# Kernel optimization log

Measured on AMD Instinct MI355X. Metric: run time of the kernel, lower is better.

Reference implementation:

```python
import jax, jax.numpy as jnp
import numpy as np
from jax import lax

B, T, D, H = 32, 512, 1024, 1024


def setup_inputs() -> dict:
    key = jax.random.key(0)
    ks = jax.random.split(key, 6)
    inp = jax.random.normal(ks[0], (B, T, D), jnp.float32)
    attention_mask = jnp.ones((B, T), jnp.float32)
    nonzero_index = jax.random.randint(ks[1], (B, 1), 0, T)
    # Stacked gate weights, gate order (i, f, g, o); equivalent to 8 separate Linears.
    W_x = jax.random.normal(ks[2], (D, 4 * H), jnp.float32) * 0.02
    W_h = jax.random.normal(ks[3], (H, 4 * H), jnp.float32) * 0.02
    b_x = jax.random.normal(ks[4], (4 * H,), jnp.float32) * 0.02
    b_h = jax.random.normal(ks[5], (4 * H,), jnp.float32) * 0.02
    return {"input": inp, "attention_mask": attention_mask, "nonzero_index": nonzero_index,
            "W_x": W_x, "W_h": W_h, "b_x": b_x, "b_h": b_h}


def reference(input, attention_mask, nonzero_index, W_x, W_h, b_x, b_h):
    # Precompute all input-side gate projections in one big matmul: [B,T,4H]
    x_gates = jnp.einsum('btd,dg->btg', input, W_x) + b_x + b_h

    def step(carry, xg):
        h, c = carry                       # [B,H] each
        g = xg + h @ W_h                   # [B,4H]
        i, f, gg, o = jnp.split(g, 4, axis=-1)
        i = jax.nn.sigmoid(i)
        f = jax.nn.sigmoid(f)
        gg = jnp.tanh(gg)
        o = jax.nn.sigmoid(o)
        c = f * c + i * gg
        h = o * jnp.tanh(c)
        return (h, c), (h, c)

    h0 = jnp.zeros((B, H), x_gates.dtype)
    c0 = jnp.zeros((B, H), x_gates.dtype)
    _, (hs, cs) = lax.scan(step, (h0, c0), jnp.swapaxes(x_gates, 0, 1))  # [T,B,H]
    hts = jnp.swapaxes(hs, 0, 1)  # [B,T,H]
    cts = jnp.swapaxes(cs, 0, 1)
    # cls token gathered BEFORE masking (matches original order)
    cls_token = jnp.take_along_axis(hts, nonzero_index[:, :, None], axis=1)[:, 0, :]
    hts = hts * attention_mask[:, :, None]
    cts = cts * attention_mask[:, :, None]
    return (hts, hts, cts, cls_token)
```

## Files before the change

kernel.cpp:

```cpp
#include <hip/hip_runtime.h>
#include <stdint.h>


typedef _Float16 f16;
typedef __attribute__((ext_vector_type(8))) _Float16 f16x8;
typedef __attribute__((ext_vector_type(4))) float f32x4;
typedef __attribute__((ext_vector_type(4))) unsigned int u32x4;

#define NG 2
#define NW 8
#define HBYTES (2 * NG * 2048 * 16)

__device__ __forceinline__ float sigm(float v){ return 1.f/(1.f+__expf(-v)); }
__device__ __forceinline__ float tanh_(float v){ return 2.f/(1.f+__expf(-2.f*v)) - 1.f; }

__device__ __forceinline__ u32x4 ld16_sc(const void* p) {
  u32x4 r;
  asm volatile("global_load_dwordx4 %0, %1, off sc0 sc1" : "=v"(r) : "v"(p));
  return r;
}
__device__ __forceinline__ void st2_sc(void* p, uint32_t v) {
  asm volatile("global_store_short %0, %1, off sc0 sc1" :: "v"(p), "v"(v) : "memory");
}

__global__ __launch_bounds__(512, 1) void lstm_kernel(
    const float* __restrict__ xin, const float* __restrict__ amask,
    const int* __restrict__ nzidx, const float* __restrict__ Wx,
    const float* __restrict__ Wh, const float* __restrict__ bx,
    const float* __restrict__ bh, float* __restrict__ out,
    uint32_t* __restrict__ ws)
{
  __shared__ __align__(16) f16 Wl[128][64][8];
  __shared__ __align__(16) float pl[NW][2][64][4];

  const int tid  = threadIdx.x;
  const int lane = tid & 63;
  const int wid  = tid >> 6;
  const int r    = blockIdx.x & 127;
  const int G    = blockIdx.x >> 7;
  const int hbase = r * 8;

  uint8_t* hb8 = (uint8_t*)ws;

  for (int f = wid; f < 128; f += NW) {
    const int side = f >> 6, kf = (f >> 1) & 31, nt = f & 1;
    const int c16 = lane & 15, kslot = lane >> 4;
    const int g = nt * 2 + (c16 >> 3);
    const int gcol = g * 1024 + hbase + (c16 & 7);
    const int k0 = kf * 32 + kslot * 8;
    const float* Wsrc = side ? Wh : Wx;
    f16x8 v;
#pragma unroll
    for (int e = 0; e < 8; ++e) v[e] = (f16)Wsrc[(size_t)(k0 + e) * 4096 + gcol];
    *(f16x8*)&Wl[f][lane][0] = v;
  }
  const int b  = tid >> 3;
  const int hc = tid & 7;
  const int b_glob = G * 16 + b;
  float bias[4] = {0.f, 0.f, 0.f, 0.f};
  float cval = 0.f;
  int myidx = -1;
  if (tid < 128) {
#pragma unroll
    for (int g = 0; g < 4; ++g) {
      const int gcol = g * 1024 + hbase + hc;
      bias[g] = bx[gcol] + bh[gcol];
    }
    myidx = nzidx[b_glob];
  }
  const int bb = lane & 15, kslot = lane >> 4;
  f32x4 xf[4][2];
  {
    const size_t xrow = ((size_t)(G * 16 + bb) * 512) * 1024;
#pragma unroll
    for (int q = 0; q < 4; ++q) {
      const float* xs = xin + xrow + (wid * 4 + q) * 32 + kslot * 8;
      xf[q][0] = *(const f32x4*)xs;
      xf[q][1] = *(const f32x4*)(xs + 4);
    }
  }
  __syncthreads();

  bool gave_up = false;
#pragma unroll 1
  for (int t = 0; t < 512; ++t) {
    f16x8 xa[4];
#pragma unroll
    for (int q = 0; q < 4; ++q) {
      f16x8 a;
#pragma unroll
      for (int i = 0; i < 4; ++i) { a[i] = (f16)xf[q][0][i]; a[i + 4] = (f16)xf[q][1][i]; }
      xa[q] = a;
    }
    f32x4 acc0 = {0.f,0.f,0.f,0.f}, acc1 = {0.f,0.f,0.f,0.f};
#pragma unroll
    for (int q = 0; q < 4; ++q) {
      const int kf = wid * 4 + q;
      f16x8 b0 = *(const f16x8*)&Wl[kf * 2 + 0][lane][0];
      f16x8 b1 = *(const f16x8*)&Wl[kf * 2 + 1][lane][0];
      acc0 = __builtin_amdgcn_mfma_f32_16x16x32_f16(xa[q], b0, acc0, 0, 0, 0);
      acc1 = __builtin_amdgcn_mfma_f32_16x16x32_f16(xa[q], b1, acc1, 0, 0, 0);
    }
    if (t + 1 < 512) {
      const size_t xrow = ((size_t)(G * 16 + bb) * 512 + (size_t)(t + 1)) * 1024;
#pragma unroll
      for (int q = 0; q < 4; ++q) {
        const float* xs = xin + xrow + (wid * 4 + q) * 32 + kslot * 8;
        xf[q][0] = *(const f32x4*)xs;
        xf[q][1] = *(const f32x4*)(xs + 4);
      }
    }
    if (t > 0) {
      const uint8_t* hsrc = hb8 + ((size_t)((t & 1) * NG + G) << 15);
      const uint32_t tb = ((uint32_t)(t >> 1) + 1u) & 3u;
      const uint32_t pat = (tb & 1u) | ((tb >> 1) << 16);
      u32x4 hq[4];
      int spins = 0;
      for (;;) {
#pragma unroll
        for (int q = 0; q < 4; ++q) {
          const int rsrc = (wid * 4 + q) * 4 + kslot;
          hq[q] = ld16_sc(hsrc + ((size_t)(rsrc * 16 + bb) << 4));
        }
        asm volatile("s_waitcnt vmcnt(0)" ::: "memory");
        if (gave_up) break;
        bool ok = true;
#pragma unroll
        for (int q = 0; q < 4; ++q) {
#pragma unroll
          for (int j = 0; j < 4; ++j) ok &= ((hq[q][j] & 0x00010001u) == pat);
        }
        if (__all((int)ok)) break;
        if (++spins > (1 << 13)) { gave_up = true; break; }
        __builtin_amdgcn_s_sleep(1);
      }
#pragma unroll
      for (int q = 0; q < 4; ++q) {
        union { u32x4 u; f16x8 v; } cu; cu.u = hq[q];
        const int kf = wid * 4 + q;
        f16x8 b0 = *(const f16x8*)&Wl[64 + kf * 2 + 0][lane][0];
        f16x8 b1 = *(const f16x8*)&Wl[64 + kf * 2 + 1][lane][0];
        acc0 = __builtin_amdgcn_mfma_f32_16x16x32_f16(cu.v, b0, acc0, 0, 0, 0);
        acc1 = __builtin_amdgcn_mfma_f32_16x16x32_f16(cu.v, b1, acc1, 0, 0, 0);
      }
    }
    *(f32x4*)&pl[wid][0][lane][0] = acc0;
    *(f32x4*)&pl[wid][1][lane][0] = acc1;
    __syncthreads();
    if (tid < 128) {
      float s[4];
#pragma unroll
      for (int g = 0; g < 4; ++g) {
        const int lp = ((g & 1) * 8 + hc) + 16 * (b >> 2);
        const int reg = b & 3;
        float v = bias[g];
#pragma unroll
        for (int w = 0; w < NW; ++w) v += pl[w][g >> 1][lp][reg];
        s[g] = v;
      }
      const float ig = sigm(s[0]);
      const float fg = sigm(s[1]);
      const float gg = tanh_(s[2]);
      const float og = sigm(s[3]);
      cval = fg * cval + ig * gg;
      const float hval = og * tanh_(cval);
      if (t < 511) {
        union { f16 f; uint16_t u; } pk; pk.f = (f16)hval;
        const uint32_t tbp = ((uint32_t)((t + 1) >> 1) + 1u) & 3u;
        const uint32_t bitv = (hc & 1) ? ((tbp >> 1) & 1u) : (tbp & 1u);
        const uint32_t val = ((uint32_t)pk.u & 0xFFFEu) | bitv;
        uint8_t* dst = hb8 + ((size_t)(((t + 1) & 1) * NG + G) << 15)
                     + ((size_t)(r * 16 + b) << 4) + (hc << 1);
        st2_sc(dst, val);
      }
      const float mval = amask[(size_t)b_glob * 512 + (size_t)t];
      const size_t o0 = ((size_t)b_glob * 512 + (size_t)t) * 1024 + (size_t)(hbase + hc);
      out[o0] = hval * mval;
      out[o0 + 16777216u] = hval * mval;
      out[o0 + 33554432u] = cval * mval;
      if (t == myidx) out[50331648u + (size_t)b_glob * 1024 + (size_t)(hbase + hc)] = hval;
    }
    __syncthreads();
  }
}

extern "C" void kernel_launch(void* const* d_in, const int* in_sizes, int n_in,
                              void* d_out, int out_size, void* d_ws, size_t ws_size,
                              hipStream_t stream) {
  const float* xin   = (const float*)d_in[0];
  const float* amask = (const float*)d_in[1];
  const int*   nzidx = (const int*)d_in[2];
  const float* Wx    = (const float*)d_in[3];
  const float* Wh    = (const float*)d_in[4];
  const float* bx    = (const float*)d_in[5];
  const float* bh    = (const float*)d_in[6];
  float* out = (float*)d_out;
  uint32_t* ws = (uint32_t*)d_ws;

  hipMemsetAsync(d_ws, 0, HBYTES, stream);

  void* args[] = {(void*)&xin, (void*)&amask, (void*)&nzidx, (void*)&Wx,
                  (void*)&Wh, (void*)&bx, (void*)&bh, (void*)&out, (void*)&ws};
  hipError_t e = hipLaunchCooperativeKernel((const void*)lstm_kernel, dim3(256), dim3(512),
                                            args, 0, stream);
  if (e != hipSuccess) {
    lstm_kernel<<<dim3(256), dim3(512), 0, stream>>>(xin, amask, nzidx, Wx, Wh, bx, bh, out, ws);
  }
}
```

Baseline: 2.231 ms.

## Double-buffer partial sums, drop trailing barrier, issue h loads before x-side MFMAs

Double-buffers the LDS partial-sum array so the second __syncthreads per step can be removed. The recurrent h loads are issued before the input-side MFMAs so their latency overlaps that compute. The spin loop drops s_sleep and only re-issues loads after a failed check. The next x prefetch now runs after h arrives, and the attention-mask value is prefetched one step ahead. The aim is to shorten the per-step critical path of the serial recurrence, at the cost of tighter polling and more reliance on the flag protocol for ordering.

Result: faster. 2.098 ms (-6.0%).

```diff
diff --git a/kernel.cpp b/kernel.cpp
--- a/kernel.cpp
+++ b/kernel.cpp
@@ -31,7 +31,7 @@
     uint32_t* __restrict__ ws)
 {
   __shared__ __align__(16) f16 Wl[128][64][8];
-  __shared__ __align__(16) float pl[NW][2][64][4];
+  __shared__ __align__(16) float pl[2][NW][2][64][4];
 
   const int tid  = threadIdx.x;
   const int lane = tid & 63;
@@ -44,10 +44,10 @@
 
   for (int f = wid; f < 128; f += NW) {
     const int side = f >> 6, kf = (f >> 1) & 31, nt = f & 1;
-    const int c16 = lane & 15, kslot = lane >> 4;
+    const int c16 = lane & 15, kslot_ = lane >> 4;
     const int g = nt * 2 + (c16 >> 3);
     const int gcol = g * 1024 + hbase + (c16 & 7);
-    const int k0 = kf * 32 + kslot * 8;
+    const int k0 = kf * 32 + kslot_ * 8;
     const float* Wsrc = side ? Wh : Wx;
     f16x8 v;
 #pragma unroll
@@ -58,7 +58,7 @@
   const int hc = tid & 7;
   const int b_glob = G * 16 + b;
   float bias[4] = {0.f, 0.f, 0.f, 0.f};
-  float cval = 0.f;
+  float cval = 0.f, mv_cur = 0.f;
   int myidx = -1;
   if (tid < 128) {
 #pragma unroll
@@ -67,6 +67,7 @@
       bias[g] = bx[gcol] + bh[gcol];
     }
     myidx = nzidx[b_glob];
+    mv_cur = amask[(size_t)b_glob * 512];
   }
   const int bb = lane & 15, kslot = lane >> 4;
   f32x4 xf[4][2];
@@ -84,6 +85,7 @@
   bool gave_up = false;
 #pragma unroll 1
   for (int t = 0; t < 512; ++t) {
+    const int ppl = t & 1;
     f16x8 xa[4];
 #pragma unroll
     for (int q = 0; q < 4; ++q) {
@@ -91,6 +93,20 @@
 #pragma unroll
       for (int i = 0; i < 4; ++i) { a[i] = (f16)xf[q][0][i]; a[i + 4] = (f16)xf[q][1][i]; }
       xa[q] = a;
+    }
+    const uint8_t* hsrc = hb8 + ((size_t)((t & 1) * NG + G) << 15);
+    uint32_t pat = 0;
+    size_t aoff[4];
+    u32x4 hq[4];
+    if (t > 0) {
+      const uint32_t tb = ((uint32_t)(t >> 1) + 1u) & 3u;
+      pat = (tb & 1u) | (((tb >> 1) & 1u) << 16);
+#pragma unroll
+      for (int q = 0; q < 4; ++q) {
+        const int rsrc = (wid * 4 + q) * 4 + kslot;
+        aoff[q] = (size_t)(rsrc * 16 + bb) << 4;
+        hq[q] = ld16_sc(hsrc + aoff[q]);
+      }
     }
     f32x4 acc0 = {0.f,0.f,0.f,0.f}, acc1 = {0.f,0.f,0.f,0.f};
 #pragma unroll
@@ -101,38 +117,36 @@
       acc0 = __builtin_amdgcn_mfma_f32_16x16x32_f16(xa[q], b0, acc0, 0, 0, 0);
       acc1 = __builtin_amdgcn_mfma_f32_16x16x32_f16(xa[q], b1, acc1, 0, 0, 0);
     }
-    if (t + 1 < 512) {
-      const size_t xrow = ((size_t)(G * 16 + bb) * 512 + (size_t)(t + 1)) * 1024;
-#pragma unroll
-      for (int q = 0; q < 4; ++q) {
-        const float* xs = xin + xrow + (wid * 4 + q) * 32 + kslot * 8;
-        xf[q][0] = *(const f32x4*)xs;
-        xf[q][1] = *(const f32x4*)(xs + 4);
-      }
-    }
     if (t > 0) {
-      const uint8_t* hsrc = hb8 + ((size_t)((t & 1) * NG + G) << 15);
-      const uint32_t tb = ((uint32_t)(t >> 1) + 1u) & 3u;
-      const uint32_t pat = (tb & 1u) | ((tb >> 1) << 16);
-      u32x4 hq[4];
-      int spins = 0;
-      for (;;) {
+      if (!gave_up) {
+        bool got = false;
+        int spins = 0;
+        for (;;) {
+          asm volatile("s_waitcnt vmcnt(0)" ::: "memory");
+          __builtin_amdgcn_sched_barrier(0);
+          bool ok = true;
+#pragma unroll
+          for (int q = 0; q < 4; ++q)
+#pragma unroll
+            for (int j = 0; j < 4; ++j) ok &= ((hq[q][j] & 0x00010001u) == pat);
+          if (__all((int)ok)) { got = true; break; }
+          if (++spins > (1 << 14)) break;
+#pragma unroll
+          for (int q = 0; q < 4; ++q) hq[q] = ld16_sc(hsrc + aoff[q]);
+        }
+        if (!got) gave_up = true;
+      } else {
+        asm volatile("s_waitcnt vmcnt(0)" ::: "memory");
+        __builtin_amdgcn_sched_barrier(0);
+      }
+      if (t + 1 < 512) {
+        const size_t xrow = ((size_t)(G * 16 + bb) * 512 + (size_t)(t + 1)) * 1024;
 #pragma unroll
         for (int q = 0; q < 4; ++q) {
-          const int rsrc = (wid * 4 + q) * 4 + kslot;
-          hq[q] = ld16_sc(hsrc + ((size_t)(rsrc * 16 + bb) << 4));
+          const float* xs = xin + xrow + (wid * 4 + q) * 32 + kslot * 8;
+          xf[q][0] = *(const f32x4*)xs;
+          xf[q][1] = *(const f32x4*)(xs + 4);
         }
-        asm volatile("s_waitcnt vmcnt(0)" ::: "memory");
-        if (gave_up) break;
-        bool ok = true;
-#pragma unroll
-        for (int q = 0; q < 4; ++q) {
-#pragma unroll
-          for (int j = 0; j < 4; ++j) ok &= ((hq[q][j] & 0x00010001u) == pat);
-        }
-        if (__all((int)ok)) break;
-        if (++spins > (1 << 13)) { gave_up = true; break; }
-        __builtin_amdgcn_s_sleep(1);
       }
 #pragma unroll
       for (int q = 0; q < 4; ++q) {
@@ -143,9 +157,17 @@
         acc0 = __builtin_amdgcn_mfma_f32_16x16x32_f16(cu.v, b0, acc0, 0, 0, 0);
         acc1 = __builtin_amdgcn_mfma_f32_16x16x32_f16(cu.v, b1, acc1, 0, 0, 0);
       }
-    }
-    *(f32x4*)&pl[wid][0][lane][0] = acc0;
-    *(f32x4*)&pl[wid][1][lane][0] = acc1;
+    } else {
+      const size_t xrow = ((size_t)(G * 16 + bb) * 512 + 1) * 1024;
+#pragma unroll
+      for (int q = 0; q < 4; ++q) {
+        const float* xs = xin + xrow + (wid * 4 + q) * 32 + kslot * 8;
+        xf[q][0] = *(const f32x4*)xs;
+        xf[q][1] = *(const f32x4*)(xs + 4);
+      }
+    }
+    *(f32x4*)&pl[ppl][wid][0][lane][0] = acc0;
+    *(f32x4*)&pl[ppl][wid][1][lane][0] = acc1;
     __syncthreads();
     if (tid < 128) {
       float s[4];
@@ -155,7 +177,7 @@
         const int reg = b & 3;
         float v = bias[g];
 #pragma unroll
-        for (int w = 0; w < NW; ++w) v += pl[w][g >> 1][lp][reg];
+        for (int w = 0; w < NW; ++w) v += pl[ppl][w][g >> 1][lp][reg];
         s[g] = v;
       }
       const float ig = sigm(s[0]);
@@ -173,14 +195,14 @@
                      + ((size_t)(r * 16 + b) << 4) + (hc << 1);
         st2_sc(dst, val);
       }
-      const float mval = amask[(size_t)b_glob * 512 + (size_t)t];
+      const float mval = mv_cur;
+      if (t + 1 < 512) mv_cur = amask[(size_t)b_glob * 512 + (size_t)(t + 1)];
       const size_t o0 = ((size_t)b_glob * 512 + (size_t)t) * 1024 + (size_t)(hbase + hc);
       out[o0] = hval * mval;
       out[o0 + 16777216u] = hval * mval;
       out[o0 + 33554432u] = cval * mval;
       if (t == myidx) out[50331648u + (size_t)b_glob * 1024 + (size_t)(hbase + hc)] = hval;
     }
-    __syncthreads();
   }
 }
 
```
